# Performance work log

Measured on AMD Instinct MI355X. Metric: run time of the kernel, lower is better.

## Reference

```python
import jax, jax.numpy as jnp
import numpy as np

B, S, D, H = 2, 2048, 1024, 16
HD = D // H
EPS = 1e-8
LN_EPS = 1e-5


def setup_inputs() -> dict:
    key = jax.random.key(0)
    ks = jax.random.split(key, 12)
    std = 0.02
    inp = {}
    inp["x"] = jax.random.normal(ks[0], (B, S, D), jnp.float32)
    # q/k/v/out projections (stored (in, out); y = x @ W + b)
    inp["Wq"] = jax.random.normal(ks[1], (D, D), jnp.float32) * std
    inp["bq"] = jnp.zeros((D,), jnp.float32)
    inp["Wk"] = jax.random.normal(ks[2], (D, D), jnp.float32) * std
    inp["bk"] = jnp.zeros((D,), jnp.float32)
    inp["Wv"] = jax.random.normal(ks[3], (D, D), jnp.float32) * std
    inp["bv"] = jnp.zeros((D,), jnp.float32)
    inp["Wo"] = jax.random.normal(ks[4], (D, D), jnp.float32) * std
    inp["bo"] = jnp.zeros((D,), jnp.float32)
    # 4 DeltaResidualBlocks stacked on axis 0: [q, k, v, out]
    inp["dWk"] = jax.random.normal(ks[5], (4, D, D), jnp.float32) * 0.01  # k_proj, no bias
    inp["dbw"] = jnp.zeros((4, D), jnp.float32)                           # beta_proj weight (init zeros)
    inp["dbb"] = jnp.full((4,), -4.0, jnp.float32)                        # beta_proj bias
    inp["dWv"] = jax.random.normal(ks[6], (4, D), jnp.float32) * 0.02     # v_proj weight (d_v=1)
    inp["dbv"] = jnp.zeros((4,), jnp.float32)                             # v_proj bias
    inp["ln_g"] = jnp.ones((D,), jnp.float32)
    inp["ln_b"] = jnp.zeros((D,), jnp.float32)
    return inp


def reference(x, Wq, bq, Wk, bk, Wv, bv, Wo, bo, dWk, dbw, dbb, dWv, dbv, ln_g, ln_b):
    def delta(h, v_in, i):
        # DeltaResidualBlock (d_v=1): h + beta * k * (v - k.h)
        k_raw = jnp.einsum('bsd,de->bse', h, dWk[i])
        k = k_raw / (jnp.linalg.norm(k_raw, axis=-1, keepdims=True) + EPS)
        beta = 2.0 * jax.nn.sigmoid(jnp.einsum('bsd,d->bs', h, dbw[i])[..., None] + dbb[i])  # (B,S,1)
        v = jnp.einsum('bsd,d->bs', v_in, dWv[i])[..., None] + dbv[i]                        # (B,S,1)
        k_dot_h = jnp.sum(k * h, axis=-1, keepdims=True)
        return h + beta * k * (v - k_dot_h)

    q = delta(x, x @ Wq + bq, 0)
    k = delta(x, x @ Wk + bk, 1)
    v = delta(x, x @ Wv + bv, 2)

    # (B,S,D) -> (B,H,S,HD)
    q = q.reshape(B, S, H, HD).transpose(0, 2, 1, 3)
    k = k.reshape(B, S, H, HD).transpose(0, 2, 1, 3)
    v = v.reshape(B, S, H, HD).transpose(0, 2, 1, 3)

    scale = HD ** -0.5
    scores = jnp.einsum('bhqd,bhkd->bhqk', q, k) * scale
    attn = jax.nn.softmax(scores, axis=-1)
    out = jnp.einsum('bhqk,bhkd->bhqd', attn, v)
    out = out.transpose(0, 2, 1, 3).reshape(B, S, D)
    out = out @ Wo + bo

    y = delta(x, out, 3)

    # LayerNorm
    mu = jnp.mean(y, axis=-1, keepdims=True)
    var = jnp.mean((y - mu) ** 2, axis=-1, keepdims=True)
    y = (y - mu) / jnp.sqrt(var + LN_EPS) * ln_g + ln_b
    return y
```

## Files before the change

### kernel.cpp

```cpp
#include <hip/hip_runtime.h>

#define BB 2
#define SS 2048
#define DD 1024
#define HH 16
#define HD 64
#define MM (BB*SS)
#define KC 4
#define KT_PER (SS/64/KC)
#define KSTEPS (DD/64)

typedef unsigned short u16;
typedef __attribute__((ext_vector_type(8))) short bf16x8;
typedef __attribute__((ext_vector_type(4))) float f32x4;

typedef __attribute__((address_space(1))) const unsigned int* gas_t;
typedef __attribute__((address_space(3))) unsigned int* las_t;

#ifndef __has_builtin
#define __has_builtin(x) 0
#endif
#if __has_builtin(__builtin_amdgcn_exp2f)
#define EXP2F(x) __builtin_amdgcn_exp2f(x)
#else
#define EXP2F(x) __expf((x)*0.6931471805599453f)
#endif
#define QSCALE 0.18033688011112042f

__device__ __forceinline__ void gl_lds16(const u16* g, u16* l){
  __builtin_amdgcn_global_load_lds((gas_t)g, (las_t)l, 16, 0, 0);
}

__device__ __forceinline__ u16 f2bf(float f){
  unsigned u = __float_as_uint(f);
  u += 0x7FFF + ((u >> 16) & 1);
  return (u16)(u >> 16);
}
__device__ __forceinline__ float bf2f(u16 h){
  return __uint_as_float(((unsigned)h) << 16);
}
__device__ __forceinline__ float dot4f(float4 a, float4 b){
  return a.x*b.x + a.y*b.y + a.z*b.z + a.w*b.w;
}

template <int CTRL>
__device__ __forceinline__ float dppadd(float x){
  int y = __builtin_amdgcn_update_dpp(0, __float_as_int(x), CTRL, 0xF, 0xF, true);
  return x + __int_as_float(y);
}
__device__ __forceinline__ float4 wsum64_f4(float4 v){
  #define DPP_ST(c) v.x=dppadd<c>(v.x); v.y=dppadd<c>(v.y); v.z=dppadd<c>(v.z); v.w=dppadd<c>(v.w);
  DPP_ST(0x111) DPP_ST(0x112) DPP_ST(0x114) DPP_ST(0x118) DPP_ST(0x142) DPP_ST(0x143)
  #undef DPP_ST
  return v;
}
__device__ __forceinline__ float2 wsum64_f2(float2 v){
  #define DPP_ST(c) v.x=dppadd<c>(v.x); v.y=dppadd<c>(v.y);
  DPP_ST(0x111) DPP_ST(0x112) DPP_ST(0x114) DPP_ST(0x118) DPP_ST(0x142) DPP_ST(0x143)
  #undef DPP_ST
  return v;
}

#define SB0() __builtin_amdgcn_sched_barrier(0)
#define SBAR() do { \
  __builtin_amdgcn_sched_barrier(0); \
  __builtin_amdgcn_s_barrier(); \
  __builtin_amdgcn_sched_barrier(0); \
} while (0)

#define NB_CONV 2048
#define NB_TRAN 1024
#define NB_PREC 4100
#define NB_PREP (NB_CONV+NB_TRAN+NB_PREC)
__global__ void prep_kernel(const float* __restrict__ x, u16* __restrict__ xb,
                            const float* __restrict__ dWk, u16* __restrict__ dWkT,
                            const float* __restrict__ Wq_, const float* __restrict__ bq_,
                            const float* __restrict__ Wk_, const float* __restrict__ bk_,
                            const float* __restrict__ Wv_, const float* __restrict__ bv_,
                            const float* __restrict__ Wo_, const float* __restrict__ bo_,
                            const float* __restrict__ dWv, const float* __restrict__ dbv,
                            float* __restrict__ wv, float* __restrict__ cv) {
  int blk = blockIdx.x, t = threadIdx.x;
  if (blk < NB_CONV) {
    size_t idx = ((size_t)blk*256 + t)*8;
    float4 a = *(const float4*)(x + idx);
    float4 b = *(const float4*)(x + idx + 4);
    union { u16 u[8]; uint4 v; } pk;
    pk.u[0]=f2bf(a.x); pk.u[1]=f2bf(a.y); pk.u[2]=f2bf(a.z); pk.u[3]=f2bf(a.w);
    pk.u[4]=f2bf(b.x); pk.u[5]=f2bf(b.y); pk.u[6]=f2bf(b.z); pk.u[7]=f2bf(b.w);
    *(uint4*)(xb + idx) = pk.v;
    return;
  }
  blk -= NB_CONV;
  if (blk < NB_TRAN) {
    int i = blk >> 8, rest = blk & 255;
    int k0 = (rest >> 4) << 6, n0 = (rest & 15) << 6;
    const float* src = dWk + (size_t)i*DD*DD;
    u16* dst = dWkT + (size_t)i*DD*DD;
    __shared__ u16 tr[64*68];
    const int krb = (t >> 4) << 2;
    const int nqb = (t & 15) << 2;
    float4 v0 = *(const float4*)(src + (size_t)(k0+krb+0)*DD + n0 + nqb);
    float4 v1 = *(const float4*)(src + (size_t)(k0+krb+1)*DD + n0 + nqb);
    float4 v2 = *(const float4*)(src + (size_t)(k0+krb+2)*DD + n0 + nqb);
    float4 v3 = *(const float4*)(src + (size_t)(k0+krb+3)*DD + n0 + nqb);
    *(uint2*)(&tr[(nqb+0)*68 + krb]) = make_uint2(
        (unsigned)f2bf(v0.x) | ((unsigned)f2bf(v1.x)<<16),
        (unsigned)f2bf(v2.x) | ((unsigned)f2bf(v3.x)<<16));
    *(uint2*)(&tr[(nqb+1)*68 + krb]) = make_uint2(
        (unsigned)f2bf(v0.y) | ((unsigned)f2bf(v1.y)<<16),
        (unsigned)f2bf(v2.y) | ((unsigned)f2bf(v3.y)<<16));
    *(uint2*)(&tr[(nqb+2)*68 + krb]) = make_uint2(
        (unsigned)f2bf(v0.z) | ((unsigned)f2bf(v1.z)<<16),
        (unsigned)f2bf(v2.z) | ((unsigned)f2bf(v3.z)<<16));
    *(uint2*)(&tr[(nqb+3)*68 + krb]) = make_uint2(
        (unsigned)f2bf(v0.w) | ((unsigned)f2bf(v1.w)<<16),
        (unsigned)f2bf(v2.w) | ((unsigned)f2bf(v3.w)<<16));
    __syncthreads();
    const int n = t >> 2, c = t & 3;
    uint2 r0 = *(uint2*)(&tr[n*68 + c*16 + 0]);
    uint2 r1 = *(uint2*)(&tr[n*68 + c*16 + 4]);
    uint2 r2 = *(uint2*)(&tr[n*68 + c*16 + 8]);
    uint2 r3 = *(uint2*)(&tr[n*68 + c*16 + 12]);
    u16* dp = dst + (size_t)(n0+n)*DD + k0 + c*16;
    *(uint4*)(dp + 0) = make_uint4(r0.x, r0.y, r1.x, r1.y);
    *(uint4*)(dp + 8) = make_uint4(r2.x, r2.y, r3.x, r3.y);
    return;
  }
  blk -= NB_TRAN;
  {
    int i = blk / 1025, row = blk % 1025;
    const float* W    = (i==0)?Wq_:(i==1)?Wk_:(i==2)?Wv_:Wo_;
    const float* bvec = (i==0)?bq_:(i==1)?bk_:(i==2)?bv_:bo_;
    const float* s = dWv + i*DD;
    __shared__ float red[256];
    float acc = 0.f;
    if (row < DD) {
      const float* r = W + (size_t)row * DD;
      for (int e = t; e < DD; e += 256) acc += r[e]*s[e];
    } else {
      for (int e = t; e < DD; e += 256) acc += bvec[e]*s[e];
    }
    red[t] = acc; __syncthreads();
    for (int off=128; off>0; off>>=1){ if(t<off) red[t]+=red[t+off]; __syncthreads(); }
    if (t==0) {
      if (row < DD) wv[i*DD + row] = red[0];
      else          cv[i] = red[0] + dbv[i];
    }
  }
}

__device__ __forceinline__ void stage_half(const u16* __restrict__ g, u16* l,
                                           int k0, int half, int isA,
                                           int wid, int lane) {
  const int lr = lane>>3, lc = lane&7;
  #pragma unroll
  for (int j=0; j<2; j++) {
    const int u = wid*2 + j;
    int grow;
    if (isA) grow = ((u & 8) ? 128 + ((u & 7)<<3) : (u<<3)) + (half<<6);
    else     grow = ((u>>2)<<6) + ((u&3)<<3) + (half<<5);
    gl_lds16(g + (size_t)(grow + lr)*DD + k0 + ((lc^lr)<<3), l + grow*64);
  }
}

__device__ __forceinline__ void lda4(const u16* base, int row0, int q15, int quad,
                                     int sw, bf16x8 (&f)[4][2]) {
  #pragma unroll
  for (int mf=0; mf<4; mf++)
    #pragma unroll
    for (int kk=0; kk<2; kk++)
      f[mf][kk] = *(const bf16x8*)(base + (row0 + mf*16 + q15)*64 + (((kk*4+quad)^sw)<<3));
}
__device__ __forceinline__ void ldb2(const u16* base, int row0, int q15, int quad,
                                     int sw, bf16x8 (&f)[2][2]) {
  #pragma unroll
  for (int nf=0; nf<2; nf++)
    #pragma unroll
    for (int kk=0; kk<2; kk++)
      f[nf][kk] = *(const bf16x8*)(base + (row0 + nf*16 + q15)*64 + (((kk*4+quad)^sw)<<3));
}
__device__ __forceinline__ void quad_mfma(const bf16x8 (&af)[4][2], const bf16x8 (&bfr)[2][2],
                                          f32x4 (&acc)[8][4], int mo, int no) {
  __builtin_amdgcn_s_setprio(1);
  #pragma unroll
  for (int kk=0; kk<2; kk++)
    #pragma unroll
    for (int mf=0; mf<4; mf++)
      #pragma unroll
      for (int nf=0; nf<2; nf++)
        acc[mo+mf][no+nf] = __builtin_amdgcn_mfma_f32_16x16x32_bf16(
            bfr[nf][kk], af[mf][kk], acc[mo+mf][no+nf], 0,0,0);
  __builtin_amdgcn_s_setprio(0);
}

__global__ __launch_bounds__(512, 2) void gemm_dwk_8ph(const u16* __restrict__ xb,
                          const u16* __restrict__ Bt, u16* __restrict__ kraw) {
  const int bid = blockIdx.x;
  const int xcd = bid & 7, rr = bid >> 3;
  const int i = xcd >> 1;
  const int mt = ((xcd & 1) << 3) | (rr & 7);
  const int ntile = rr >> 3;
  const int m0 = mt << 8, n0 = ntile << 8;
  const u16* Ab = xb + (size_t)m0*DD;
  const u16* Bb = Bt + (size_t)i*DD*DD + (size_t)n0*DD;
  u16* C = kraw + (size_t)i*MM*DD;

  const int t = threadIdx.x, wid = t>>6, lane = t&63;
  const int q15 = lane&15, quad = lane>>4, sw = q15&7;
  const int wm = wid>>2, wn = wid&3;
  const int arow = wm<<7, brow = wn<<6;

  __shared__ u16 As[2][256*64];
  __shared__ u16 Bs[2][256*64];

  f32x4 acc[8][4];
  #pragma unroll
  for (int a=0;a<8;a++)
    #pragma unroll
    for (int b2=0;b2<4;b2++) acc[a][b2] = (f32x4){0.f,0.f,0.f,0.f};

  stage_half(Ab, As[0], 0,  0, 1, wid, lane);
  stage_half(Bb, Bs[0], 0,  0, 0, wid, lane);
  stage_half(Bb, Bs[0], 0,  1, 0, wid, lane);
  stage_half(Ab, As[0], 0,  1, 1, wid, lane);
  stage_half(Ab, As[1], 64, 0, 1, wid, lane);
  stage_half(Bb, Bs[1], 64, 0, 0, wid, lane);
  stage_half(Bb, Bs[1], 64, 1, 0, wid, lane);
  SB0();
  asm volatile("s_waitcnt vmcnt(6)" ::: "memory");
  SBAR();

  for (int u=0; u<KSTEPS; ++u) {
    const int cur = u & 1;
    const u16* Ac = As[cur]; const u16* Bc = Bs[cur];
    const int k1 = (u+1 < KSTEPS ? u+1 : KSTEPS-1) << 6;
    const int k2 = (u+2 < KSTEPS ? u+2 : KSTEPS-1) << 6;
    bf16x8 a0[4][2], a1[4][2], b0[2][2], b1[2][2];

    lda4(Ac, arow,    q15, quad, sw, a0);
    ldb2(Bc, brow,    q15, quad, sw, b0);
    ldb2(Bc, brow+32, q15, quad, sw, b1);
    stage_half(Ab, As[cur^1], k1, 1, 1, wid, lane);
    SB0();
    quad_mfma(a0, b0, acc, 0, 0);
    quad_mfma(a0, b1, acc, 0, 2);
    SB0();
    lda4(Ac, arow+64, q15, quad, sw, a1);
    SB0();
    __builtin_amdgcn_s_barrier();
    SB0();
    stage_half(Ab, As[cur], k2, 0, 1, wid, lane);
    stage_half(Bb, Bs[cur], k2, 0, 0, wid, lane);
    stage_half(Bb, Bs[cur], k2, 1, 0, wid, lane);
    SB0();
    quad_mfma(a1, b1, acc, 4, 2);
    quad_mfma(a1, b0, acc, 4, 0);
    SB0();
    asm volatile("s_waitcnt vmcnt(6)" ::: "memory");
    __builtin_amdgcn_s_barrier();
    SB0();
  }

  #pragma unroll
  for (int mf=0; mf<8; mf++) {
    const int m = m0 + arow + mf*16 + q15;
    u16* Crow = C + (size_t)m*DD + n0 + brow;
    #pragma unroll
    for (int nf=0; nf<4; nf++) {
      unsigned u0 = (unsigned)f2bf(acc[mf][nf][0]) | ((unsigned)f2bf(acc[mf][nf][1]) << 16);
      unsigned u1 = (unsigned)f2bf(acc[mf][nf][2]) | ((unsigned)f2bf(acc[mf][nf][3]) << 16);
      *(uint2*)(Crow + nf*16 + quad*4) = make_uint2(u0, u1);
    }
  }
}

__global__ void delta_qkv_kernel(const float* __restrict__ x, const u16* __restrict__ kraw,
                                 const float* __restrict__ dbw, const float* __restrict__ dbb,
                                 const float* __restrict__ wv, const float* __restrict__ cv,
                                 u16* __restrict__ qk, float* __restrict__ Vw) {
  int m = blockIdx.x, t = threadIdx.x, w = t>>6, lane = t&63;
  const float* xr = x + (size_t)m*DD;
  float4 xv = *(const float4*)(xr + t*4);
  __shared__ float4 part[3][4];
  float4 kvs[3];
  #pragma unroll
  for (int i=0;i<3;i++) {
    ushort4 ku = *(const ushort4*)(kraw + (size_t)i*MM*DD + (size_t)m*DD + t*4);
    float4 kv = make_float4(bf2f(ku.x), bf2f(ku.y), bf2f(ku.z), bf2f(ku.w));
    kvs[i] = kv;
    float4 bwv = *(const float4*)(dbw + i*DD + t*4);
    float4 wvv = *(const float4*)(wv  + i*DD + t*4);
    float4 red = make_float4(dot4f(kv,kv), dot4f(kv,xv), dot4f(xv,bwv), dot4f(xv,wvv));
    red = wsum64_f4(red);
    if (lane==63) part[i][w] = red;
  }
  __syncthreads();
  float cc[3];
  #pragma unroll
  for (int i=0;i<3;i++) {
    float4 r0=part[i][0], r1=part[i][1], r2=part[i][2], r3=part[i][3];
    float s0=r0.x+r1.x+r2.x+r3.x, s1=r0.y+r1.y+r2.y+r3.y;
    float s2=r0.z+r1.z+r2.z+r3.z, s3=r0.w+r1.w+r2.w+r3.w;
    float nrmE = sqrtf(s0) + 1e-8f;
    float kdh  = s1 / nrmE;
    float beta = 2.f / (1.f + __expf(-(s2 + dbb[i])));
    float vs   = s3 + cv[i];
    cc[i] = beta * (vs - kdh) / nrmE;
  }
  {
    float c = cc[0]; float4 kv = kvs[0];
    ushort4 ou;
    ou.x = f2bf((xv.x + c*kv.x)*QSCALE); ou.y = f2bf((xv.y + c*kv.y)*QSCALE);
    ou.z = f2bf((xv.z + c*kv.z)*QSCALE); ou.w = f2bf((xv.w + c*kv.w)*QSCALE);
    *(ushort4*)(qk + (size_t)m*DD + t*4) = ou;
  }
  {
    float c = cc[1]; float4 kv = kvs[1];
    ushort4 ou;
    ou.x = f2bf(xv.x + c*kv.x); ou.y = f2bf(xv.y + c*kv.y);
    ou.z = f2bf(xv.z + c*kv.z); ou.w = f2bf(xv.w + c*kv.w);
    *(ushort4*)(qk + (size_t)MM*DD + (size_t)m*DD + t*4) = ou;
  }
  {
    float c = cc[2]; float4 kv = kvs[2];
    float4 vv = make_float4(xv.x + c*kv.x, xv.y + c*kv.y, xv.z + c*kv.z, xv.w + c*kv.w);
    float4 w3 = *(const float4*)(wv + 3*DD + t*4);
    float s = dot4f(vv, w3);
    #pragma unroll
    for (int off=1; off<16; off<<=1) s += __shfl_xor(s, off);
    if ((lane & 15) == 0) {
      int head = t >> 4;
      int b = m >> 11, srow = m & (SS-1);
      Vw[((size_t)(b*HH + head))*SS + srow] = s;
    }
  }
}

__global__ __launch_bounds__(256, 4) void flash_mfma(const u16* __restrict__ qb,
     const u16* __restrict__ kb, const float* __restrict__ Vw,
     float* __restrict__ l_arr, float* __restrict__ pv_arr) {
  const int qt = blockIdx.x, h = blockIdx.y;
  const int b = blockIdx.z >> 2, kc = blockIdx.z & 3;
  const int t = threadIdx.x, w = t>>6, lane = t&63, q15 = lane&15, quad = lane>>4;
  const int lr = lane>>3, lc = lane&7, gsw = lc ^ lr;
  const int sw = q15 & 7;
  __shared__ u16 Ks[3][64*64];
  __shared__ float Vws[KT_PER*64];
  __shared__ float2 red2[4*64];
  const size_t hb = (size_t)h*HD;
  const u16* kbase = kb + (size_t)(b*SS + kc*KT_PER*64)*DD + hb;
  const float* vwb = Vw + (size_t)(b*HH + h)*SS + kc*KT_PER*64;

  bf16x8 qf[4][2];
  #pragma unroll
  for (int qt2=0; qt2<4; qt2++) {
    const u16* qrow = qb + (size_t)(b*SS + qt*64 + qt2*16 + q15)*DD + hb;
    qf[qt2][0] = *(const bf16x8*)(qrow + quad*8);
    qf[qt2][1] = *(const bf16x8*)(qrow + 32 + quad*8);
  }
  if (t < KT_PER*64/4) {
    float4 v = *(const float4*)(vwb + t*4);
    *(float4*)(&Vws[t*4]) = v;
  }
  #pragma unroll
  for (int j=0; j<2; j++) {
    int r = (w*2+j)*8 + lr;
    gl_lds16(kbase + (size_t)r*DD + gsw*8, &Ks[0][((w*2+j)*8)*64]);
    gl_lds16(kbase + (size_t)(64 + r)*DD + gsw*8, &Ks[1][((w*2+j)*8)*64]);
  }
  float l_acc[4] = {0.f,0.f,0.f,0.f}, pv_acc[4] = {0.f,0.f,0.f,0.f};
  __syncthreads();

  #pragma unroll
  for (int kt=0; kt<KT_PER; kt++) {
    if (kt+2 < KT_PER) {
      #pragma unroll
      for (int j=0; j<2; j++) {
        int r = (w*2+j)*8 + lr;
        gl_lds16(kbase + (size_t)((kt+2)*64 + r)*DD + gsw*8,
                 &Ks[(kt+2)%3][((w*2+j)*8)*64]);
      }
    }
    bf16x8 kf0 = *(bf16x8*)(&Ks[kt%3][(w*16+q15)*64 + ((quad  )^sw)*8]);
    bf16x8 kf1 = *(bf16x8*)(&Ks[kt%3][(w*16+q15)*64 + ((4+quad)^sw)*8]);
    f32x4 Sacc[4];
    #pragma unroll
    for (int qt2=0; qt2<4; qt2++) Sacc[qt2] = (f32x4){0.f,0.f,0.f,0.f};
    #pragma unroll
    for (int qt2=0; qt2<4; qt2++) {
      Sacc[qt2] = __builtin_amdgcn_mfma_f32_16x16x32_bf16(kf0, qf[qt2][0], Sacc[qt2], 0,0,0);
      Sacc[qt2] = __builtin_amdgcn_mfma_f32_16x16x32_bf16(kf1, qf[qt2][1], Sacc[qt2], 0,0,0);
    }
    float4 va = *(const float4*)(&Vws[kt*64 + w*16 + quad*4]);
    #pragma unroll
    for (int qt2=0; qt2<4; qt2++) {
      float p0 = EXP2F(fminf(Sacc[qt2][0], 30.f));
      float p1 = EXP2F(fminf(Sacc[qt2][1], 30.f));
      float p2 = EXP2F(fminf(Sacc[qt2][2], 30.f));
      float p3 = EXP2F(fminf(Sacc[qt2][3], 30.f));
      l_acc[qt2]  += (p0 + p1) + (p2 + p3);
      pv_acc[qt2] += p0*va.x + p1*va.y + p2*va.z + p3*va.w;
    }
    if (kt < KT_PER-1) {
      __builtin_amdgcn_sched_barrier(0);
      if (kt+2 < KT_PER) asm volatile("s_waitcnt vmcnt(2)" ::: "memory");
      else               asm volatile("s_waitcnt vmcnt(0)" ::: "memory");
      __builtin_amdgcn_s_barrier();
      __builtin_amdgcn_sched_barrier(0);
    }
  }
  #pragma unroll
  for (int qt2=0; qt2<4; qt2++) {
    l_acc[qt2]  += __shfl_xor(l_acc[qt2], 16);  l_acc[qt2]  += __shfl_xor(l_acc[qt2], 32);
    pv_acc[qt2] += __shfl_xor(pv_acc[qt2], 16); pv_acc[qt2] += __shfl_xor(pv_acc[qt2], 32);
  }
  if (lane < 16) {
    #pragma unroll
    for (int qt2=0; qt2<4; qt2++)
      red2[w*64 + qt2*16 + lane] = make_float2(l_acc[qt2], pv_acc[qt2]);
  }
  __syncthreads();
  if (t < 64) {
    float2 p0 = red2[t], p1 = red2[64+t], p2 = red2[128+t], p3 = red2[192+t];
    float ls = (p0.x+p1.x) + (p2.x+p3.x);
    float ps = (p0.y+p1.y) + (p2.y+p3.y);
    int tok = b*SS + qt*64 + t;
    size_t idx = ((size_t)kc*MM + tok)*HH + h;
    l_arr[idx]  = ls;
    pv_arr[idx] = ps;
  }
}

__global__ void final_kernel(const float* __restrict__ x, const u16* __restrict__ kraw3,
                             const float* __restrict__ l_arr, const float* __restrict__ pv_arr,
                             const float* __restrict__ dbw, const float* __restrict__ dbb,
                             const float* __restrict__ cv,
                             const float* __restrict__ ln_g, const float* __restrict__ ln_b,
                             float* __restrict__ out) {
  int m = blockIdx.x, t = threadIdx.x, w = t>>6, lane = t&63;
  const float* xr = x     + (size_t)m*DD;
  const u16*   kr = kraw3 + (size_t)m*DD;
  float4 xv  = *(const float4*)(xr + t*4);
  ushort4 ku = *(const ushort4*)(kr + t*4);
  float4 kv  = make_float4(bf2f(ku.x), bf2f(ku.y), bf2f(ku.z), bf2f(ku.w));
  float4 bwv = *(const float4*)(dbw + 3*DD + t*4);
  __shared__ float4 part[4];
  __shared__ float2 part2[4];
  __shared__ float v3s;
  if (t < 16) {
    float lsum = 0.f, psum = 0.f;
    #pragma unroll
    for (int kc=0; kc<KC; kc++) {
      size_t idx = ((size_t)kc*MM + m)*HH + t;
      lsum += l_arr[idx];
      psum += pv_arr[idx];
    }
    float val = psum / lsum;
    #pragma unroll
    for (int off=1; off<16; off<<=1) val += __shfl_xor(val, off);
    if (t==0) v3s = val;
  }
  float4 red = make_float4(dot4f(kv,kv), dot4f(kv,xv), dot4f(xv,bwv), 0.f);
  red = wsum64_f4(red);
  if (lane==63) part[w] = red;
  __syncthreads();
  float4 r0=part[0], r1=part[1], r2=part[2], r3=part[3];
  float s0=r0.x+r1.x+r2.x+r3.x, s1=r0.y+r1.y+r2.y+r3.y, s2=r0.z+r1.z+r2.z+r3.z;
  float nrmE = sqrtf(s0) + 1e-8f;
  float kdh  = s1 / nrmE;
  float beta = 2.f / (1.f + __expf(-(s2 + dbb[3])));
  float v3   = v3s + cv[3];
  float c = beta * (v3 - kdh) / nrmE;
  float y0 = xv.x + c*kv.x, y1 = xv.y + c*kv.y, y2 = xv.z + c*kv.z, y3 = xv.w + c*kv.w;
  float2 rr = make_float2(y0+y1+y2+y3, y0*y0+y1*y1+y2*y2+y3*y3);
  rr = wsum64_f2(rr);
  if (lane==63) part2[w] = rr;
  __syncthreads();
  float ssum = part2[0].x+part2[1].x+part2[2].x+part2[3].x;
  float ssq  = part2[0].y+part2[1].y+part2[2].y+part2[3].y;
  float mu   = ssum * (1.f/DD);
  float var  = ssq * (1.f/DD) - mu*mu;
  float rstd = rsqrtf(var + 1e-5f);
  float4 g  = *(const float4*)(ln_g + t*4);
  float4 bb = *(const float4*)(ln_b + t*4);
  float4 ov;
  ov.x = (y0-mu)*rstd*g.x + bb.x;
  ov.y = (y1-mu)*rstd*g.y + bb.y;
  ov.z = (y2-mu)*rstd*g.z + bb.z;
  ov.w = (y3-mu)*rstd*g.w + bb.w;
  *(float4*)(out + (size_t)m*DD + t*4) = ov;
}

extern "C" void kernel_launch(void* const* d_in, const int* in_sizes, int n_in,
                              void* d_out, int out_size, void* d_ws, size_t ws_size,
                              hipStream_t stream) {
  const float* x    = (const float*)d_in[0];
  const float* Wq_  = (const float*)d_in[1];
  const float* bq_  = (const float*)d_in[2];
  const float* Wk_  = (const float*)d_in[3];
  const float* bk_  = (const float*)d_in[4];
  const float* Wv_  = (const float*)d_in[5];
  const float* bv_  = (const float*)d_in[6];
  const float* Wo_  = (const float*)d_in[7];
  const float* bo_  = (const float*)d_in[8];
  const float* dWk  = (const float*)d_in[9];
  const float* dbw  = (const float*)d_in[10];
  const float* dbb  = (const float*)d_in[11];
  const float* dWv  = (const float*)d_in[12];
  const float* dbv  = (const float*)d_in[13];
  const float* ln_g = (const float*)d_in[14];
  const float* ln_b = (const float*)d_in[15];
  float* out = (float*)d_out;
  char* WS = (char*)d_ws;

  float* wv     = (float*)WS;
  float* cv     = (float*)(WS + 16384);
  u16*   kraw   = (u16*)  (WS + 16640);
  u16*   qk     = (u16*)  (WS + 16640 + (size_t)4*MM*DD*2);
  u16*   dWkT   = (u16*)  (WS + 16640 + (size_t)6*MM*DD*2);
  u16*   xb     = (u16*)  (WS + 16640 + (size_t)6*MM*DD*2 + (size_t)4*DD*DD*2);
  char*  tail   = WS + 16640 + (size_t)6*MM*DD*2 + (size_t)8*DD*DD*2;
  float* Vw     = (float*)tail;
  float* l_arr  = (float*)(tail + (size_t)BB*HH*SS*4);
  float* pv_arr = (float*)(tail + (size_t)BB*HH*SS*4 + (size_t)KC*MM*HH*4);

  prep_kernel<<<NB_PREP, 256, 0, stream>>>(
      x, xb, dWk, dWkT, Wq_,bq_,Wk_,bk_,Wv_,bv_,Wo_,bo_, dWv, dbv, wv, cv);
  gemm_dwk_8ph<<<256, 512, 0, stream>>>(xb, dWkT, kraw);
  delta_qkv_kernel<<<MM, 256, 0, stream>>>(x, kraw, dbw, dbb, wv, cv, qk, Vw);
  flash_mfma<<<dim3(SS/64, HH, BB*KC), 256, 0, stream>>>(
      qk, qk + (size_t)MM*DD, Vw, l_arr, pv_arr);
  final_kernel<<<MM, 256, 0, stream>>>(x, kraw + 3*(size_t)MM*DD, l_arr, pv_arr,
                                       dbw, dbb, cv, ln_g, ln_b, out);
}
```

Before: 263.3 us.

## Load K tiles directly into registers per wave, dropping LDS staging and barriers

The flash attention kernel no longer stages K tiles and V weights through triple-buffered LDS with block-wide barriers. Each wave now loads its own 32-key K fragments and V-weight slices straight from global memory into registers, double-buffered in registers across four iterations. This removes LDS traffic and __syncthreads stalls, at the cost of uncoalesced strided global loads, higher register pressure, and a launch-bounds occupancy hint lowered from 4 to 2.

```diff
diff --git a/kernel.cpp b/kernel.cpp
--- a/kernel.cpp
+++ b/kernel.cpp
@@ -8,6 +8,7 @@
 #define MM (BB*SS)
 #define KC 4
 #define KT_PER (SS/64/KC)
+#define NTT 16
 #define KSTEPS (DD/64)
 
 typedef unsigned short u16;
@@ -337,16 +338,12 @@
   }
 }
 
-__global__ __launch_bounds__(256, 4) void flash_mfma(const u16* __restrict__ qb,
+__global__ __launch_bounds__(256, 2) void flash_mfma(const u16* __restrict__ qb,
      const u16* __restrict__ kb, const float* __restrict__ Vw,
      float* __restrict__ l_arr, float* __restrict__ pv_arr) {
   const int qt = blockIdx.x, h = blockIdx.y;
   const int b = blockIdx.z >> 2, kc = blockIdx.z & 3;
   const int t = threadIdx.x, w = t>>6, lane = t&63, q15 = lane&15, quad = lane>>4;
-  const int lr = lane>>3, lc = lane&7, gsw = lc ^ lr;
-  const int sw = q15 & 7;
-  __shared__ u16 Ks[3][64*64];
-  __shared__ float Vws[KT_PER*64];
   __shared__ float2 red2[4*64];
   const size_t hb = (size_t)h*HD;
   const u16* kbase = kb + (size_t)(b*SS + kc*KT_PER*64)*DD + hb;
@@ -359,56 +356,56 @@
     qf[qt2][0] = *(const bf16x8*)(qrow + quad*8);
     qf[qt2][1] = *(const bf16x8*)(qrow + 32 + quad*8);
   }
-  if (t < KT_PER*64/4) {
-    float4 v = *(const float4*)(vwb + t*4);
-    *(float4*)(&Vws[t*4]) = v;
-  }
-  #pragma unroll
-  for (int j=0; j<2; j++) {
-    int r = (w*2+j)*8 + lr;
-    gl_lds16(kbase + (size_t)r*DD + gsw*8, &Ks[0][((w*2+j)*8)*64]);
-    gl_lds16(kbase + (size_t)(64 + r)*DD + gsw*8, &Ks[1][((w*2+j)*8)*64]);
-  }
   float l_acc[4] = {0.f,0.f,0.f,0.f}, pv_acc[4] = {0.f,0.f,0.f,0.f};
-  __syncthreads();
-
-  #pragma unroll
-  for (int kt=0; kt<KT_PER; kt++) {
-    if (kt+2 < KT_PER) {
-      #pragma unroll
-      for (int j=0; j<2; j++) {
-        int r = (w*2+j)*8 + lr;
-        gl_lds16(kbase + (size_t)((kt+2)*64 + r)*DD + gsw*8,
-                 &Ks[(kt+2)%3][((w*2+j)*8)*64]);
+
+  bf16x8 c00, c01, c10, c11; float4 cva0, cva1;
+  {
+    const u16* kr = kbase + (size_t)(w*32 + q15)*DD + quad*8;
+    c00 = *(const bf16x8*)(kr);
+    c01 = *(const bf16x8*)(kr + 32);
+    c10 = *(const bf16x8*)(kr + 16*DD);
+    c11 = *(const bf16x8*)(kr + 16*DD + 32);
+    cva0 = *(const float4*)(vwb + w*32 + quad*4);
+    cva1 = *(const float4*)(vwb + w*32 + 16 + quad*4);
+  }
+  #pragma unroll
+  for (int j=0; j<4; ++j) {
+    bf16x8 n00, n01, n10, n11; float4 nva0, nva1;
+    if (j < 3) {
+      const int ktn = (j+1)*4 + w;
+      const u16* kr = kbase + (size_t)(ktn*32 + q15)*DD + quad*8;
+      n00 = *(const bf16x8*)(kr);
+      n01 = *(const bf16x8*)(kr + 32);
+      n10 = *(const bf16x8*)(kr + 16*DD);
+      n11 = *(const bf16x8*)(kr + 16*DD + 32);
+      nva0 = *(const float4*)(vwb + ktn*32 + quad*4);
+      nva1 = *(const float4*)(vwb + ktn*32 + 16 + quad*4);
+    }
+    #pragma unroll
+    for (int qt2=0; qt2<4; qt2++) {
+      f32x4 S0 = (f32x4){0.f,0.f,0.f,0.f}, S1 = (f32x4){0.f,0.f,0.f,0.f};
+      S0 = __builtin_amdgcn_mfma_f32_16x16x32_bf16(c00, qf[qt2][0], S0, 0,0,0);
+      S0 = __builtin_amdgcn_mfma_f32_16x16x32_bf16(c01, qf[qt2][1], S0, 0,0,0);
+      S1 = __builtin_amdgcn_mfma_f32_16x16x32_bf16(c10, qf[qt2][0], S1, 0,0,0);
+      S1 = __builtin_amdgcn_mfma_f32_16x16x32_bf16(c11, qf[qt2][1], S1, 0,0,0);
+      {
+        float p0 = EXP2F(fminf(S0[0], 30.f));
+        float p1 = EXP2F(fminf(S0[1], 30.f));
+        float p2 = EXP2F(fminf(S0[2], 30.f));
+        float p3 = EXP2F(fminf(S0[3], 30.f));
+        l_acc[qt2]  += (p0 + p1) + (p2 + p3);
+        pv_acc[qt2] += p0*cva0.x + p1*cva0.y + p2*cva0.z + p3*cva0.w;
       }
-    }
-    bf16x8 kf0 = *(bf16x8*)(&Ks[kt%3][(w*16+q15)*64 + ((quad  )^sw)*8]);
-    bf16x8 kf1 = *(bf16x8*)(&Ks[kt%3][(w*16+q15)*64 + ((4+quad)^sw)*8]);
-    f32x4 Sacc[4];
-    #pragma unroll
-    for (int qt2=0; qt2<4; qt2++) Sacc[qt2] = (f32x4){0.f,0.f,0.f,0.f};
-    #pragma unroll
-    for (int qt2=0; qt2<4; qt2++) {
-      Sacc[qt2] = __builtin_amdgcn_mfma_f32_16x16x32_bf16(kf0, qf[qt2][0], Sacc[qt2], 0,0,0);
-      Sacc[qt2] = __builtin_amdgcn_mfma_f32_16x16x32_bf16(kf1, qf[qt2][1], Sacc[qt2], 0,0,0);
-    }
-    float4 va = *(const float4*)(&Vws[kt*64 + w*16 + quad*4]);
-    #pragma unroll
-    for (int qt2=0; qt2<4; qt2++) {
-      float p0 = EXP2F(fminf(Sacc[qt2][0], 30.f));
-      float p1 = EXP2F(fminf(Sacc[qt2][1], 30.f));
-      float p2 = EXP2F(fminf(Sacc[qt2][2], 30.f));
-      float p3 = EXP2F(fminf(Sacc[qt2][3], 30.f));
-      l_acc[qt2]  += (p0 + p1) + (p2 + p3);
-      pv_acc[qt2] += p0*va.x + p1*va.y + p2*va.z + p3*va.w;
-    }
-    if (kt < KT_PER-1) {
-      __builtin_amdgcn_sched_barrier(0);
-      if (kt+2 < KT_PER) asm volatile("s_waitcnt vmcnt(2)" ::: "memory");
-      else               asm volatile("s_waitcnt vmcnt(0)" ::: "memory");
-      __builtin_amdgcn_s_barrier();
-      __builtin_amdgcn_sched_barrier(0);
-    }
+      {
+        float p0 = EXP2F(fminf(S1[0], 30.f));
+        float p1 = EXP2F(fminf(S1[1], 30.f));
+        float p2 = EXP2F(fminf(S1[2], 30.f));
+        float p3 = EXP2F(fminf(S1[3], 30.f));
+        l_acc[qt2]  += (p0 + p1) + (p2 + p3);
+        pv_acc[qt2] += p0*cva1.x + p1*cva1.y + p2*cva1.z + p3*cva1.w;
+      }
+    }
+    if (j < 3) { c00=n00; c01=n01; c10=n10; c11=n11; cva0=nva0; cva1=nva1; }
   }
   #pragma unroll
   for (int qt2=0; qt2<4; qt2++) {
```

After: 243.8 us. -7.4%, faster.
